# Kernel tuning notes

Hardware: AMD Instinct MI355X
Metric: run time of the kernel (lower is better)

Reference implementation:

```python
import jax, jax.numpy as jnp
import numpy as np

CUBIC_A = -0.75  # torch bicubic coefficient


def _cubic_weights(t):
    # torch get_cubic_upsample_coefficients, t in [0,1): weights for taps at -1,0,1,2
    A = CUBIC_A
    def c1(x):
        return ((A + 2.0) * x - (A + 3.0)) * x * x + 1.0
    def c2(x):
        return ((A * x - 5.0 * A) * x + 8.0 * A) * x - 4.0 * A
    return jnp.stack([c2(t + 1.0), c1(t), c1(1.0 - t), c2(2.0 - t)])  # [4, ...]


def geo_cyclic_pad(x, p):
    # GeoCyclicPadding: pole rows are flipped and shifted by half the longitudes,
    # longitude is padded cyclically.
    B, C, H, W = x.shape
    top = jnp.roll(jnp.flip(x[:, :, :p, :], axis=2), W // 2, axis=3)
    bot = jnp.roll(jnp.flip(x[:, :, H - p:, :], axis=2), W // 2, axis=3)
    x = jnp.concatenate([top, x, bot], axis=2)
    x = jnp.concatenate([x[:, :, :, -p:], x, x[:, :, :, :p]], axis=3)
    return x


def bicubic_grid_sample(img, gx, gy):
    # img: [N, Hp, Wp]; gx, gy: [N, Ho, Wo] normalized coords in [-1, 1]
    # torch grid_sample(mode='bicubic', align_corners=True, padding_mode='border')
    N, Hp, Wp = img.shape
    ix = (gx + 1.0) * 0.5 * (Wp - 1)
    iy = (gy + 1.0) * 0.5 * (Hp - 1)
    ix0 = jnp.floor(ix)
    iy0 = jnp.floor(iy)
    tx = ix - ix0
    ty = iy - iy0
    wx = _cubic_weights(tx)  # [4, N, Ho, Wo]
    wy = _cubic_weights(ty)  # [4, N, Ho, Wo]
    offs = jnp.arange(-1, 3, dtype=jnp.int32)[:, None, None, None]
    xs = jnp.clip(ix0.astype(jnp.int32)[None] + offs, 0, Wp - 1)  # [4,N,Ho,Wo] (border)
    ys = jnp.clip(iy0.astype(jnp.int32)[None] + offs, 0, Hp - 1)
    n = jnp.arange(N, dtype=jnp.int32)[None, None, :, None, None]
    vals = img[n, ys[:, None], xs[None, :]]  # [4, 4, N, Ho, Wo]
    return jnp.einsum('jnhw,inhw,jinhw->nhw', wy, wx, vals)


def reference(hidden_features, lat_grid, lon_grid, W_vel, b_vel, dt):
    B, C, H, W = hidden_features.shape
    two_pi = 2.0 * jnp.pi
    # velocity net (pointwise conv hidden_dim -> 2*hidden_dim)
    vel = jnp.einsum('bchw,oc->bohw', hidden_features, W_vel) + b_vel[None, :, None, None]
    vel = vel.reshape(B, 2, C, H, W)
    u, v = vel[:, 0], vel[:, 1]
    lon_prime = -u * dt
    lat_prime = -v * dt
    lat_p = lat_grid[:, None]  # [B,1,H,W] broadcasts over C
    lon_p = lon_grid[:, None]
    # rotated -> standard lat/lon
    slp, clp = jnp.sin(lat_prime), jnp.cos(lat_prime)
    slo, clo = jnp.sin(lon_prime), jnp.cos(lon_prime)
    sp, cp = jnp.sin(lat_p), jnp.cos(lat_p)
    sin_lat = slp * cp + clp * clo * sp
    lat = jnp.arcsin(jnp.clip(sin_lat, -1.0 + 1e-7, 1.0 - 1e-7))
    num = clp * slo
    den = clp * clo * cp - slp * sp
    lon = jnp.remainder(lon_p + jnp.arctan2(num, den) + two_pi, two_pi)
    min_lat, max_lat = jnp.min(lat_grid), jnp.max(lat_grid)
    min_lon, max_lon = jnp.min(lon_grid), jnp.max(lon_grid)
    gx = 2.0 * (lon - min_lon) / (max_lon - min_lon) - 1.0
    gy = 2.0 * (lat - min_lat) / (max_lat - min_lat) - 1.0
    # periodic wrap in longitude, pole reflection in latitude
    gx = jnp.remainder(gx + 1.0, 2.0) - 1.0
    left = gx <= 0.0
    outer = jnp.abs(gy) > 1.0
    gx = jnp.where(outer & left, gx + 1.0, gx)
    gx = jnp.where(outer & (~left), gx - 1.0, gx)
    gy = jnp.where(gy < -1.0, -(2.0 + gy), gy)
    gy = jnp.where(gy > 1.0, 2.0 - gy, gy)
    # pad and rescale grid to padded size (align_corners=True)
    padded = geo_cyclic_pad(hidden_features, 1)  # [B,C,H+2,W+2]
    Hp, Wp = H + 2, W + 2
    gx = gx * (W / Wp)
    gy = gy * (H / Hp)
    img = padded.reshape(B * C, Hp, Wp)
    out = bicubic_grid_sample(img, gx.reshape(B * C, H, W), gy.reshape(B * C, H, W))
    return out.reshape(B, C, H, W)


def setup_inputs() -> dict:
    key = jax.random.key(0)
    k1, k2 = jax.random.split(key, 2)
    B, C, H, W = 2, 64, 180, 360
    hidden_features = jax.random.normal(k1, (B, C, H, W), dtype=jnp.float32)
    lat = jnp.linspace(-jnp.pi / 2, jnp.pi / 2, H, dtype=jnp.float32)
    lon = jnp.arange(W, dtype=jnp.float32) * (2.0 * jnp.pi / W)
    lat_grid = jnp.broadcast_to(lat[:, None], (H, W))
    lon_grid = jnp.broadcast_to(lon[None, :], (H, W))
    lat_grid = jnp.broadcast_to(lat_grid[None], (B, H, W)).astype(jnp.float32)
    lon_grid = jnp.broadcast_to(lon_grid[None], (B, H, W)).astype(jnp.float32)
    W_vel = jax.random.normal(k2, (2 * C, C), dtype=jnp.float32) * 0.02
    b_vel = jnp.zeros((2 * C,), dtype=jnp.float32)
    return {"hidden_features": hidden_features, "lat_grid": lat_grid,
            "lon_grid": lon_grid, "W_vel": W_vel, "b_vel": b_vel, "dt": 1.0}
```

## Files before the change

### kernel.cpp

```cpp
#include <hip/hip_runtime.h>
#include <math.h>

constexpr int B_ = 2, C_ = 64, H_ = 180, W_ = 360;
constexpr int HW = H_ * W_;
constexpr int Hp = H_ + 2, Wp = W_ + 2;
constexpr int O_ = 2 * C_;

typedef float float4a __attribute__((ext_vector_type(4), aligned(4)));

__device__ __forceinline__ float frem(float x, float y) {
    return x - floorf(x / y) * y;
}
__device__ __forceinline__ float frem2(float x) {
    return x - floorf(x * 0.5f) * 2.0f;
}

__device__ __forceinline__ float cub1(float x) {
    return (1.25f * x - 2.25f) * x * x + 1.0f;
}
__device__ __forceinline__ float cub2(float x) {
    return ((-0.75f * x + 3.75f) * x - 6.0f) * x + 3.0f;
}

__device__ __forceinline__ float fetch_pad(const float* __restrict__ img, int y, int x) {
    int wc = x - 1;
    if (x == 0)      wc = W_ - 1;
    if (x == Wp - 1) wc = 0;
    int hh = y - 1;
    bool top = (y == 0), bot = (y == Hp - 1);
    if (top) hh = 0;
    if (bot) hh = H_ - 1;
    if (top || bot) { wc += W_ / 2; if (wc >= W_) wc -= W_; }
    return img[hh * W_ + wc];
}

struct Coord { float tx, ty; int jx, jy; };

__device__ __forceinline__ Coord compute_coord(
    float u, float v, float dt, float sp, float cp, float lon_p,
    float min_lat, float min_lon, float inv_dlat, float inv_dlon)
{
    const float two_pi = 6.28318530717958647f;
    const float sxw = (float)W_ / (float)Wp;
    const float syh = (float)H_ / (float)Hp;

    const float lon_pr = -u * dt;
    const float lat_pr = -v * dt;
    float slp, clp, slo, clo;
    __sincosf(lat_pr, &slp, &clp);
    __sincosf(lon_pr, &slo, &clo);
    float sin_lat = slp * cp + clp * clo * sp;
    sin_lat = fminf(fmaxf(sin_lat, -1.0f + 1e-7f), 1.0f - 1e-7f);
    const float lat = asinf(sin_lat);
    const float num = clp * slo;
    const float den = clp * clo * cp - slp * sp;
    const float lon = frem(lon_p + atan2f(num, den) + two_pi, two_pi);

    float gx = (lon - min_lon) * inv_dlon - 1.0f;
    float gy = (lat - min_lat) * inv_dlat - 1.0f;
    gx = frem2(gx + 1.0f) - 1.0f;
    const bool left  = (gx <= 0.0f);
    const bool outer = (fabsf(gy) > 1.0f);
    if (outer) gx += left ? 1.0f : -1.0f;
    if (gy < -1.0f)     gy = -(2.0f + gy);
    else if (gy > 1.0f) gy = 2.0f - gy;
    gx *= sxw;
    gy *= syh;

    const float ix = (gx + 1.0f) * 0.5f * (float)(Wp - 1);
    const float iy = (gy + 1.0f) * 0.5f * (float)(Hp - 1);
    const float fx0 = floorf(ix), fy0 = floorf(iy);
    Coord cr;
    cr.tx = ix - fx0; cr.ty = iy - fy0;
    cr.jx = (int)fx0; cr.jy = (int)fy0;
    return cr;
}

__device__ __forceinline__ bool is_interior(const Coord& cr) {
    return (cr.jx >= 2) & (cr.jx <= Wp - 4) & (cr.jy >= 2) & (cr.jy <= Hp - 4);
}

__device__ __forceinline__ float bicubic_reduce(const float* t, float tx, float ty) {
    const float wx0 = cub2(tx + 1.0f), wx1 = cub1(tx);
    const float wx2 = cub1(1.0f - tx), wx3 = cub2(2.0f - tx);
    const float wy0 = cub2(ty + 1.0f), wy1 = cub1(ty);
    const float wy2 = cub1(1.0f - ty), wy3 = cub2(2.0f - ty);
    const float r0 = fmaf(wx3, t[3],  fmaf(wx2, t[2],  fmaf(wx1, t[1],  wx0 * t[0])));
    const float r1 = fmaf(wx3, t[7],  fmaf(wx2, t[6],  fmaf(wx1, t[5],  wx0 * t[4])));
    const float r2 = fmaf(wx3, t[11], fmaf(wx2, t[10], fmaf(wx1, t[9],  wx0 * t[8])));
    const float r3 = fmaf(wx3, t[15], fmaf(wx2, t[14], fmaf(wx1, t[13], wx0 * t[12])));
    return fmaf(wy3, r3, fmaf(wy2, r2, fmaf(wy1, r1, wy0 * r0)));
}

__device__ __forceinline__ void taps_interior(const float* __restrict__ img,
                                              const Coord& cr, float* t) {
    const float* __restrict__ p = img + (cr.jy - 2) * W_ + (cr.jx - 2);
#pragma unroll
    for (int r = 0; r < 4; ++r) {
        const float4a row = *(const float4a*)(p + r * W_);
        t[r * 4 + 0] = row.x; t[r * 4 + 1] = row.y;
        t[r * 4 + 2] = row.z; t[r * 4 + 3] = row.w;
    }
}

__device__ __forceinline__ void taps_border(const float* __restrict__ img,
                                            const Coord& cr, float* t) {
    int xs[4], ys[4];
#pragma unroll
    for (int r = 0; r < 4; ++r) {
        xs[r] = min(max(cr.jx - 1 + r, 0), Wp - 1);
        ys[r] = min(max(cr.jy - 1 + r, 0), Hp - 1);
    }
#pragma unroll
    for (int r = 0; r < 4; ++r)
#pragma unroll
        for (int cc = 0; cc < 4; ++cc)
            t[r * 4 + cc] = fetch_pad(img, ys[r], xs[cc]);
}

__device__ __forceinline__ float advect_one(
    const float* __restrict__ img, float u, float v, float dt,
    float sp, float cp, float lon_p,
    float min_lat, float min_lon, float inv_dlat, float inv_dlon)
{
    const Coord cr = compute_coord(u, v, dt, sp, cp, lon_p,
                                   min_lat, min_lon, inv_dlat, inv_dlon);
    float t[16];
    if (__all(is_interior(cr))) taps_interior(img, cr, t);
    else                        taps_border(img, cr, t);
    return bicubic_reduce(t, cr.tx, cr.ty);
}

constexpr int P1_PXT = 256;
constexpr int P1_OG  = 2;
constexpr int P1_OPG = O_ / P1_OG;
constexpr int P1_TILES = (HW + P1_PXT - 1) / P1_PXT;

__global__ __launch_bounds__(P1_PXT, 4) void nsl_vel(
    const float* __restrict__ hidden, const float* __restrict__ W_vel,
    const float* __restrict__ b_vel, float* __restrict__ uv)
{
    const int bid  = blockIdx.x;
    const int tile = bid % P1_TILES;
    const int og   = (bid / P1_TILES) % P1_OG;
    const int b    = bid / (P1_TILES * P1_OG);
    const int px   = tile * P1_PXT + threadIdx.x;
    if (px >= HW) return;

    float acc[P1_OPG];
#pragma unroll
    for (int j = 0; j < P1_OPG; ++j) acc[j] = b_vel[og * P1_OPG + j];

    const float* hb = hidden + (size_t)b * C_ * HW + px;
    const float* Wg = W_vel + (size_t)og * P1_OPG * C_;

    float xf[4];
#pragma unroll
    for (int t = 0; t < 4; ++t) xf[t] = hb[(size_t)t * HW];

    for (int k0 = 0; k0 < C_; k0 += 4) {
        float xc[4];
#pragma unroll
        for (int t = 0; t < 4; ++t) xc[t] = xf[t];
        if (k0 + 4 < C_) {
#pragma unroll
            for (int t = 0; t < 4; ++t) xf[t] = hb[(size_t)(k0 + 4 + t) * HW];
        }
#pragma unroll
        for (int j = 0; j < P1_OPG; ++j) {
            const float* wr = Wg + (size_t)j * C_ + k0;
            acc[j] = fmaf(wr[0], xc[0], acc[j]);
            acc[j] = fmaf(wr[1], xc[1], acc[j]);
            acc[j] = fmaf(wr[2], xc[2], acc[j]);
            acc[j] = fmaf(wr[3], xc[3], acc[j]);
        }
    }

    float* o = uv + ((size_t)b * O_ + og * P1_OPG) * HW + px;
#pragma unroll
    for (int j = 0; j < P1_OPG; ++j) o[(size_t)j * HW] = acc[j];
}

constexpr int P2_TX = 16, P2_TY = 16;
constexpr int P2_GX = (W_ + P2_TX - 1) / P2_TX;
constexpr int P2_GY = (H_ + P2_TY - 1) / P2_TY;
constexpr int P2_NTILE = P2_GX * P2_GY;
constexpr int NXCD = 8;
constexpr int BC_PER_XCD = (B_ * C_) / NXCD;

__global__ __launch_bounds__(256, 8) void nsl_advect_x(
    const float* __restrict__ hidden,
    const float* __restrict__ lat_grid,
    const float* __restrict__ lon_grid,
    const float* __restrict__ uv,
    const float* __restrict__ dt_p,
    float* __restrict__ out)
{
    const int id   = blockIdx.x;
    const int xcd  = id & (NXCD - 1);
    const int slot = id >> 3;
    const int bcl  = slot / P2_NTILE;
    const int tile = slot - bcl * P2_NTILE;
    const int bc   = xcd * BC_PER_XCD + bcl;
    const int txx  = tile % P2_GX;
    const int tyy  = tile / P2_GX;

    const int lane = threadIdx.x & 63;
    const int wv   = threadIdx.x >> 6;
    const int lx   = lane & 15;
    const int ly   = (lane >> 4) + wv * 4;
    const int px   = txx * P2_TX + lx;
    const int py   = tyy * P2_TY + ly;
    if (px >= W_ || py >= H_) return;
    const int pix  = py * W_ + px;

    const int b  = bc >> 6;
    const int c  = bc & (C_ - 1);

    const float dt      = dt_p[0];
    const float min_lat = lat_grid[0];
    const float max_lat = lat_grid[(H_ - 1) * W_];
    const float min_lon = lon_grid[0];
    const float max_lon = lon_grid[W_ - 1];
    const float inv_dlat = 2.0f / (max_lat - min_lat);
    const float inv_dlon = 2.0f / (max_lon - min_lon);

    const float lat_p = lat_grid[(size_t)b * HW + pix];
    const float lon_p = lon_grid[(size_t)b * HW + pix];
    float sp, cp;
    __sincosf(lat_p, &sp, &cp);

    const float u = uv[((size_t)b * O_ + c) * HW + pix];
    const float v = uv[((size_t)b * O_ + C_ + c) * HW + pix];

    const float* __restrict__ img = hidden + (size_t)bc * HW;
    out[(size_t)bc * HW + pix] = advect_one(img, u, v, dt, sp, cp, lon_p,
                                            min_lat, min_lon, inv_dlat, inv_dlon);
}

constexpr int FB_CG = 4, FB_CPT = C_ / FB_CG, FB_PXT = 256;
constexpr int FB_TILES = (HW + FB_PXT - 1) / FB_PXT;

__global__ __launch_bounds__(FB_PXT, 6) void nsl_fused(
    const float* __restrict__ hidden, const float* __restrict__ lat_grid,
    const float* __restrict__ lon_grid, const float* __restrict__ W_vel,
    const float* __restrict__ b_vel, const float* __restrict__ dt_p,
    float* __restrict__ out)
{
    const int bid  = blockIdx.x;
    const int tile = bid % FB_TILES;
    const int cg   = (bid / FB_TILES) % FB_CG;
    const int b    = bid / (FB_TILES * FB_CG);
    const int px   = tile * FB_PXT + threadIdx.x;
    if (px >= HW) return;

    const float dt      = dt_p[0];
    const float min_lat = lat_grid[0];
    const float max_lat = lat_grid[(H_ - 1) * W_];
    const float min_lon = lon_grid[0];
    const float max_lon = lon_grid[W_ - 1];
    const float inv_dlat = 2.0f / (max_lat - min_lat);
    const float inv_dlon = 2.0f / (max_lon - min_lon);

    const float lat_p = lat_grid[(size_t)b * HW + px];
    const float lon_p = lon_grid[(size_t)b * HW + px];
    float sp, cp;
    __sincosf(lat_p, &sp, &cp);

    float u[FB_CPT], v[FB_CPT];
#pragma unroll
    for (int i = 0; i < FB_CPT; ++i) {
        u[i] = b_vel[cg * FB_CPT + i];
        v[i] = b_vel[C_ + cg * FB_CPT + i];
    }
    const float* hb = hidden + (size_t)b * C_ * HW + px;
#pragma unroll 2
    for (int k = 0; k < C_; ++k) {
        const float x = hb[(size_t)k * HW];
#pragma unroll
        for (int i = 0; i < FB_CPT; ++i) {
            u[i] = fmaf(W_vel[(size_t)(cg * FB_CPT + i) * C_ + k], x, u[i]);
            v[i] = fmaf(W_vel[(size_t)(C_ + cg * FB_CPT + i) * C_ + k], x, v[i]);
        }
    }

    for (int i = 0; i < FB_CPT; ++i) {
        const int c = cg * FB_CPT + i;
        const float* __restrict__ img = hidden + ((size_t)b * C_ + c) * HW;
        out[((size_t)b * C_ + c) * HW + px] =
            advect_one(img, u[i], v[i], dt, sp, cp, lon_p,
                       min_lat, min_lon, inv_dlat, inv_dlon);
    }
}

extern "C" void kernel_launch(void* const* d_in, const int* in_sizes, int n_in,
                              void* d_out, int out_size, void* d_ws, size_t ws_size,
                              hipStream_t stream) {
    const float* hidden   = (const float*)d_in[0];
    const float* lat_grid = (const float*)d_in[1];
    const float* lon_grid = (const float*)d_in[2];
    const float* W_vel    = (const float*)d_in[3];
    const float* b_vel    = (const float*)d_in[4];
    const float* dt_p     = (const float*)d_in[5];
    float* out = (float*)d_out;

    const size_t uv_bytes = (size_t)B_ * O_ * HW * sizeof(float);
    if (ws_size >= uv_bytes) {
        float* uv = (float*)d_ws;
        nsl_vel<<<B_ * P1_OG * P1_TILES, P1_PXT, 0, stream>>>(hidden, W_vel, b_vel, uv);
        const int grid2 = NXCD * BC_PER_XCD * P2_NTILE;
        nsl_advect_x<<<grid2, 256, 0, stream>>>(
            hidden, lat_grid, lon_grid, uv, dt_p, out);
    } else {
        nsl_fused<<<B_ * FB_CG * FB_TILES, FB_PXT, 0, stream>>>(
            hidden, lat_grid, lon_grid, W_vel, b_vel, dt_p, out);
    }
}
```

Measured before the change: 207.1 us.

## Fuse velocity projection into tiled advection kernel, drop uv workspace

Removes the separate velocity kernel and the uv workspace. Each advection thread now computes its own u and v by a 64-channel dot product over hidden features, reading 16 channels at a time. This saves one launch and the uv write/read round trip. In exchange, every output channel rereads all 64 input channels at that pixel, so cache-level load traffic grows by a large factor.

```diff
diff --git a/kernel.cpp b/kernel.cpp
--- a/kernel.cpp
+++ b/kernel.cpp
@@ -131,56 +131,6 @@
     return bicubic_reduce(t, cr.tx, cr.ty);
 }
 
-constexpr int P1_PXT = 256;
-constexpr int P1_OG  = 2;
-constexpr int P1_OPG = O_ / P1_OG;
-constexpr int P1_TILES = (HW + P1_PXT - 1) / P1_PXT;
-
-__global__ __launch_bounds__(P1_PXT, 4) void nsl_vel(
-    const float* __restrict__ hidden, const float* __restrict__ W_vel,
-    const float* __restrict__ b_vel, float* __restrict__ uv)
-{
-    const int bid  = blockIdx.x;
-    const int tile = bid % P1_TILES;
-    const int og   = (bid / P1_TILES) % P1_OG;
-    const int b    = bid / (P1_TILES * P1_OG);
-    const int px   = tile * P1_PXT + threadIdx.x;
-    if (px >= HW) return;
-
-    float acc[P1_OPG];
-#pragma unroll
-    for (int j = 0; j < P1_OPG; ++j) acc[j] = b_vel[og * P1_OPG + j];
-
-    const float* hb = hidden + (size_t)b * C_ * HW + px;
-    const float* Wg = W_vel + (size_t)og * P1_OPG * C_;
-
-    float xf[4];
-#pragma unroll
-    for (int t = 0; t < 4; ++t) xf[t] = hb[(size_t)t * HW];
-
-    for (int k0 = 0; k0 < C_; k0 += 4) {
-        float xc[4];
-#pragma unroll
-        for (int t = 0; t < 4; ++t) xc[t] = xf[t];
-        if (k0 + 4 < C_) {
-#pragma unroll
-            for (int t = 0; t < 4; ++t) xf[t] = hb[(size_t)(k0 + 4 + t) * HW];
-        }
-#pragma unroll
-        for (int j = 0; j < P1_OPG; ++j) {
-            const float* wr = Wg + (size_t)j * C_ + k0;
-            acc[j] = fmaf(wr[0], xc[0], acc[j]);
-            acc[j] = fmaf(wr[1], xc[1], acc[j]);
-            acc[j] = fmaf(wr[2], xc[2], acc[j]);
-            acc[j] = fmaf(wr[3], xc[3], acc[j]);
-        }
-    }
-
-    float* o = uv + ((size_t)b * O_ + og * P1_OPG) * HW + px;
-#pragma unroll
-    for (int j = 0; j < P1_OPG; ++j) o[(size_t)j * HW] = acc[j];
-}
-
 constexpr int P2_TX = 16, P2_TY = 16;
 constexpr int P2_GX = (W_ + P2_TX - 1) / P2_TX;
 constexpr int P2_GY = (H_ + P2_TY - 1) / P2_TY;
@@ -188,11 +138,12 @@
 constexpr int NXCD = 8;
 constexpr int BC_PER_XCD = (B_ * C_) / NXCD;
 
-__global__ __launch_bounds__(256, 8) void nsl_advect_x(
+__global__ __launch_bounds__(256, 6) void nsl_fused_x(
     const float* __restrict__ hidden,
     const float* __restrict__ lat_grid,
     const float* __restrict__ lon_grid,
-    const float* __restrict__ uv,
+    const float* __restrict__ W_vel,
+    const float* __restrict__ b_vel,
     const float* __restrict__ dt_p,
     float* __restrict__ out)
 {
@@ -214,8 +165,8 @@
     if (px >= W_ || py >= H_) return;
     const int pix  = py * W_ + px;
 
-    const int b  = bc >> 6;
-    const int c  = bc & (C_ - 1);
+    const int b = bc >> 6;
+    const int c = bc & (C_ - 1);
 
     const float dt      = dt_p[0];
     const float min_lat = lat_grid[0];
@@ -230,67 +181,28 @@
     float sp, cp;
     __sincosf(lat_p, &sp, &cp);
 
-    const float u = uv[((size_t)b * O_ + c) * HW + pix];
-    const float v = uv[((size_t)b * O_ + C_ + c) * HW + pix];
+    const float* __restrict__ wu = W_vel + (size_t)c * C_;
+    const float* __restrict__ wvp = W_vel + (size_t)(C_ + c) * C_;
+    const float* hbp = hidden + (size_t)b * C_ * HW + pix;
+
+    float u = b_vel[c];
+    float v = b_vel[C_ + c];
+#pragma unroll 1
+    for (int k0 = 0; k0 < C_; k0 += 16) {
+        float xk[16];
+#pragma unroll
+        for (int t = 0; t < 16; ++t)
+            xk[t] = hbp[(size_t)(k0 + t) * HW];
+#pragma unroll
+        for (int t = 0; t < 16; ++t) {
+            u = fmaf(wu[k0 + t],  xk[t], u);
+            v = fmaf(wvp[k0 + t], xk[t], v);
+        }
+    }
 
     const float* __restrict__ img = hidden + (size_t)bc * HW;
     out[(size_t)bc * HW + pix] = advect_one(img, u, v, dt, sp, cp, lon_p,
                                             min_lat, min_lon, inv_dlat, inv_dlon);
-}
-
-constexpr int FB_CG = 4, FB_CPT = C_ / FB_CG, FB_PXT = 256;
-constexpr int FB_TILES = (HW + FB_PXT - 1) / FB_PXT;
-
-__global__ __launch_bounds__(FB_PXT, 6) void nsl_fused(
-    const float* __restrict__ hidden, const float* __restrict__ lat_grid,
-    const float* __restrict__ lon_grid, const float* __restrict__ W_vel,
-    const float* __restrict__ b_vel, const float* __restrict__ dt_p,
-    float* __restrict__ out)
-{
-    const int bid  = blockIdx.x;
-    const int tile = bid % FB_TILES;
-    const int cg   = (bid / FB_TILES) % FB_CG;
-    const int b    = bid / (FB_TILES * FB_CG);
-    const int px   = tile * FB_PXT + threadIdx.x;
-    if (px >= HW) return;
-
-    const float dt      = dt_p[0];
-    const float min_lat = lat_grid[0];
-    const float max_lat = lat_grid[(H_ - 1) * W_];
-    const float min_lon = lon_grid[0];
-    const float max_lon = lon_grid[W_ - 1];
-    const float inv_dlat = 2.0f / (max_lat - min_lat);
-    const float inv_dlon = 2.0f / (max_lon - min_lon);
-
-    const float lat_p = lat_grid[(size_t)b * HW + px];
-    const float lon_p = lon_grid[(size_t)b * HW + px];
-    float sp, cp;
-    __sincosf(lat_p, &sp, &cp);
-
-    float u[FB_CPT], v[FB_CPT];
-#pragma unroll
-    for (int i = 0; i < FB_CPT; ++i) {
-        u[i] = b_vel[cg * FB_CPT + i];
-        v[i] = b_vel[C_ + cg * FB_CPT + i];
-    }
-    const float* hb = hidden + (size_t)b * C_ * HW + px;
-#pragma unroll 2
-    for (int k = 0; k < C_; ++k) {
-        const float x = hb[(size_t)k * HW];
-#pragma unroll
-        for (int i = 0; i < FB_CPT; ++i) {
-            u[i] = fmaf(W_vel[(size_t)(cg * FB_CPT + i) * C_ + k], x, u[i]);
-            v[i] = fmaf(W_vel[(size_t)(C_ + cg * FB_CPT + i) * C_ + k], x, v[i]);
-        }
-    }
-
-    for (int i = 0; i < FB_CPT; ++i) {
-        const int c = cg * FB_CPT + i;
-        const float* __restrict__ img = hidden + ((size_t)b * C_ + c) * HW;
-        out[((size_t)b * C_ + c) * HW + px] =
-            advect_one(img, u[i], v[i], dt, sp, cp, lon_p,
-                       min_lat, min_lon, inv_dlat, inv_dlon);
-    }
 }
 
 extern "C" void kernel_launch(void* const* d_in, const int* in_sizes, int n_in,
@@ -304,15 +216,7 @@
     const float* dt_p     = (const float*)d_in[5];
     float* out = (float*)d_out;
 
-    const size_t uv_bytes = (size_t)B_ * O_ * HW * sizeof(float);
-    if (ws_size >= uv_bytes) {
-        float* uv = (float*)d_ws;
-        nsl_vel<<<B_ * P1_OG * P1_TILES, P1_PXT, 0, stream>>>(hidden, W_vel, b_vel, uv);
-        const int grid2 = NXCD * BC_PER_XCD * P2_NTILE;
-        nsl_advect_x<<<grid2, 256, 0, stream>>>(
-            hidden, lat_grid, lon_grid, uv, dt_p, out);
-    } else {
-        nsl_fused<<<B_ * FB_CG * FB_TILES, FB_PXT, 0, stream>>>(
-            hidden, lat_grid, lon_grid, W_vel, b_vel, dt_p, out);
-    }
-}
+    const int grid = NXCD * BC_PER_XCD * P2_NTILE;
+    nsl_fused_x<<<grid, 256, 0, stream>>>(
+        hidden, lat_grid, lon_grid, W_vel, b_vel, dt_p, out);
+}
```

Result: slower. 498.4 us (+140.7%).
